# Kernel optimization log

Hardware: AMD Instinct MI355X
Metric: run time of the kernel (lower is better)

## Reference

```python
import jax, jax.numpy as jnp
import numpy as np

D_G, D_2D, D_3D = 512, 768, 1024
D_F, RANK, ATTN_H = 256, 16, 512
B = 8192


def _xavier(key, shape):
    fan_out, fan_in = shape
    lim = float(np.sqrt(6.0 / (fan_in + fan_out)))
    return jax.random.uniform(key, shape, jnp.float32, -lim, lim)


def setup_inputs() -> dict:
    key = jax.random.key(0)
    ks = jax.random.split(key, 12)
    inp = {
        "h_g": jax.random.normal(ks[0], (B, D_G), jnp.float32),
        "h_2d": jax.random.normal(ks[1], (B, D_2D), jnp.float32),
        "h_3d": jax.random.normal(ks[2], (B, D_3D), jnp.float32),
        # modality projections (torch Linear: y = x @ W.T + b)
        "Wg": _xavier(ks[3], (D_F, D_G)),   "bg": jnp.zeros((D_F,), jnp.float32),
        "W2": _xavier(ks[4], (D_F, D_2D)),  "b2": jnp.zeros((D_F,), jnp.float32),
        "W3": _xavier(ks[5], (D_F, D_3D)),  "b3": jnp.zeros((D_F,), jnp.float32),
        # LayerNorm affine params
        "ln_g_w": jnp.ones((D_F,), jnp.float32),  "ln_g_b": jnp.zeros((D_F,), jnp.float32),
        "ln_2_w": jnp.ones((D_F,), jnp.float32),  "ln_2_b": jnp.zeros((D_F,), jnp.float32),
        "ln_3_w": jnp.ones((D_F,), jnp.float32),  "ln_3_b": jnp.zeros((D_F,), jnp.float32),
        # rank expansions (no bias)
        "U": _xavier(ks[6], (RANK * D_F, D_F)),
        "V": _xavier(ks[7], (RANK * D_F, D_F)),
        "S": _xavier(ks[8], (RANK * D_F, D_F)),
        # attention MLP
        "Wa1": _xavier(ks[9], (ATTN_H, D_G + D_2D + D_3D)), "ba1": jnp.zeros((ATTN_H,), jnp.float32),
        "Wa2": _xavier(ks[10], (RANK, ATTN_H)),             "ba2": jnp.zeros((RANK,), jnp.float32),
    }
    return inp


def _layernorm(x, w, b, eps=1e-5):
    mu = jnp.mean(x, axis=-1, keepdims=True)
    var = jnp.var(x, axis=-1, keepdims=True)
    return (x - mu) * jax.lax.rsqrt(var + eps) * w + b


def reference(h_g, h_2d, h_3d, Wg, bg, W2, b2, W3, b3,
              ln_g_w, ln_g_b, ln_2_w, ln_2_b, ln_3_w, ln_3_b,
              U, V, S, Wa1, ba1, Wa2, ba2):
    # proj + LN + ReLU (dropout=0 / eval mode)
    g = jax.nn.relu(_layernorm(h_g @ Wg.T + bg, ln_g_w, ln_g_b))
    d2 = jax.nn.relu(_layernorm(h_2d @ W2.T + b2, ln_2_w, ln_2_b))
    d3 = jax.nn.relu(_layernorm(h_3d @ W3.T + b3, ln_3_w, ln_3_b))
    b = g.shape[0]
    # rank expansion: (B, R, d_f)
    g_r = (g @ U.T).reshape(b, RANK, D_F)
    d2_r = (d2 @ V.T).reshape(b, RANK, D_F)
    d3_r = (d3 @ S.T).reshape(b, RANK, D_F)
    z_r = g_r * d2_r * d3_r  # elementwise tri-linear product
    # rank attention from raw modality concat
    h_cat = jnp.concatenate([h_g, h_2d, h_3d], axis=-1)
    beta = jax.nn.softmax(jax.nn.relu(h_cat @ Wa1.T + ba1) @ Wa2.T + ba2, axis=-1)  # (B, R)
    z = jnp.einsum('brd,br->bd', z_r, beta)  # (B, d_f)
    return z
```

## Files before the change

kernel.cpp:

```cpp
#include <hip/hip_runtime.h>
#include <stdint.h>

#define B_ROWS 8192
#define DG 512
#define D2 768
#define D3 1024
#define DCAT 2304
#define DF 256
#define RANK 16
#define AH 512

#define OFF_WG 0
#define OFF_W2 131072
#define OFF_W3 327680
#define OFF_U  589824
#define OFF_V  1638400
#define OFF_S  2686976
#define OFF_WA1 3735552

#define WS_WBUF  0u
#define WS_GBUF  9830400u
#define WS_A1P   22413312u
#define WS_ZPART 22413312u
#define WS_BETA  55967744u
#define WS_REQUIRED 94240768u

typedef __attribute__((ext_vector_type(8))) short short8;
typedef __attribute__((ext_vector_type(4))) float f32x4;

__device__ inline unsigned short f2bf(float f) {
  union { float f; unsigned int u; } v; v.f = f;
  unsigned int u = v.u + 0x7fffu + ((v.u >> 16) & 1u);
  return (unsigned short)(u >> 16);
}
__device__ inline float bf2f(unsigned short h) {
  union { float f; unsigned int u; } v; v.u = ((unsigned int)h) << 16;
  return v.f;
}

typedef const unsigned int __attribute__((address_space(1)))* as1_u32p;
typedef unsigned int __attribute__((address_space(3)))* as3_u32p;

__device__ inline void g2l16(const unsigned short* g, unsigned short* l) {
  __builtin_amdgcn_global_load_lds((as1_u32p)g, (as3_u32p)l, 16, 0, 0);
}


__global__ __launch_bounds__(256) void cvt_w_k(const float* __restrict__ Wg,
                                               const float* __restrict__ W2,
                                               const float* __restrict__ W3,
                                               const float* __restrict__ U,
                                               const float* __restrict__ V,
                                               const float* __restrict__ S,
                                               const float* __restrict__ Wa1,
                                               unsigned short* __restrict__ wbuf) {
  const int e = (blockIdx.x * 256 + threadIdx.x) * 4;
  const float* src;
  if (e < OFF_W2)       src = Wg  + e;
  else if (e < OFF_W3)  src = W2  + (e - OFF_W2);
  else if (e < OFF_U)   src = W3  + (e - OFF_W3);
  else if (e < OFF_V)   src = U   + (e - OFF_U);
  else if (e < OFF_S)   src = V   + (e - OFF_V);
  else if (e < OFF_WA1) src = S   + (e - OFF_S);
  else                  src = Wa1 + (e - OFF_WA1);
  float4 v = *(const float4*)src;
  ushort4 o;
  o.x = f2bf(v.x); o.y = f2bf(v.y); o.z = f2bf(v.z); o.w = f2bf(v.w);
  *(ushort4*)(wbuf + e) = o;
}


__global__ __launch_bounds__(512, 2) void fatgemm256_k(const float* __restrict__ hgf,
                                                       const float* __restrict__ h2f,
                                                       const float* __restrict__ h3f,
                                                       const unsigned short* __restrict__ wbuf,
                                                       const float* __restrict__ bg,
                                                       const float* __restrict__ b2,
                                                       const float* __restrict__ b3,
                                                       const float* __restrict__ wg,
                                                       const float* __restrict__ wbg,
                                                       const float* __restrict__ w2,
                                                       const float* __restrict__ wb2,
                                                       const float* __restrict__ w3,
                                                       const float* __restrict__ wb3,
                                                       unsigned short* __restrict__ gout,
                                                       unsigned short* __restrict__ a1part) {
  __shared__ __align__(16) unsigned short lA[2 * 256 * 64];
  __shared__ __align__(16) unsigned short lB[2 * 256 * 64];
  const int bid = blockIdx.x;
  const int tid = threadIdx.x;
  const int lane = tid & 63;
  const int wid = tid >> 6;
  const int wr = wid >> 2;
  const int wc = wid & 3;
  const int row_s = tid >> 3;
  const int kc_s = (((tid & 7) ^ (row_s & 7)) << 3);
  const int mbase = wr * 128 + (lane & 15);
  const int nbase = wc * 64 + (lane & 15);
  const int kq = lane >> 4;
  const int h = lane & 7;

  int role_a1 = 0, half = 0, m0 = 0, n0 = 0, z = 0, nt = 0;
  if (bid < 128)      { role_a1 = 1; half = bid >> 6; int r6 = bid & 63;
                        n0 = (r6 & 1) << 8; m0 = (r6 >> 1) << 8; nt = 18; }
  else if (bid < 160) { z = 2; m0 = (bid - 128) << 8; nt = 16; }
  else if (bid < 192) { z = 1; m0 = (bid - 160) << 8; nt = 12; }
  else                { z = 0; m0 = (bid - 192) << 8; nt = 8; }

  const float* projA = (z == 0) ? hgf : ((z == 1) ? h2f : h3f);
  const int Kz   = (z == 0) ? DG : ((z == 1) ? D2 : D3);
  const int woff = (z == 0) ? OFF_WG : ((z == 1) ? OFF_W2 : OFF_W3);

  float4 ar[8];
  auto loadA = [&](int t) {
    const float* Ag; int lda; int ka;
    if (role_a1) {
      const int tt = half * 18 + t;
      if (tt < 8)       { Ag = hgf; lda = DG; ka = tt * 64; }
      else if (tt < 20) { Ag = h2f; lda = D2; ka = (tt - 8) * 64; }
      else              { Ag = h3f; lda = D3; ka = (tt - 20) * 64; }
      Ag += (size_t)m0 * lda;
    } else {
      lda = Kz; Ag = projA + (size_t)m0 * lda; ka = t * 64;
    }
#pragma unroll
    for (int q = 0; q < 4; ++q) {
      const float* src = Ag + (size_t)(q * 64 + row_s) * lda + ka + kc_s;
      ar[q * 2]     = *(const float4*)src;
      ar[q * 2 + 1] = *(const float4*)(src + 4);
    }
  };

  auto writeA = [&](unsigned short* dA) {
#pragma unroll
    for (int q = 0; q < 4; ++q) {
      const float4 a = ar[q * 2], b = ar[q * 2 + 1];
      short8 w;
      w[0] = (short)f2bf(a.x); w[1] = (short)f2bf(a.y);
      w[2] = (short)f2bf(a.z); w[3] = (short)f2bf(a.w);
      w[4] = (short)f2bf(b.x); w[5] = (short)f2bf(b.y);
      w[6] = (short)f2bf(b.z); w[7] = (short)f2bf(b.w);
      *(short8*)(dA + (q * 512 + tid) * 8) = w;
    }
  };

  auto stageB = [&](int t, unsigned short* dB) {
    const unsigned short* Bg; int ldb; int kb;
    if (role_a1) {
      const int tt = half * 18 + t;
      Bg = wbuf + OFF_WA1 + (size_t)n0 * DCAT; ldb = DCAT; kb = tt * 64;
    } else {
      Bg = wbuf + woff; ldb = Kz; kb = t * 64;
    }
#pragma unroll
    for (int q = 0; q < 4; ++q)
      g2l16(Bg + (size_t)(q * 64 + row_s) * ldb + kb + kc_s, dB + (q * 512 + tid) * 8);
  };

  f32x4 acc[8][4];
#pragma unroll
  for (int ti = 0; ti < 8; ++ti)
#pragma unroll
    for (int tj = 0; tj < 4; ++tj)
      acc[ti][tj] = (f32x4){0.f, 0.f, 0.f, 0.f};

  auto compute = [&](const unsigned short* sA, const unsigned short* sB) {
#pragma unroll
    for (int kk = 0; kk < 2; ++kk) {
      const int kch = (kk << 2) + kq;
      const int ko = ((kch ^ h) << 3);
      short8 af[8], bfr[4];
#pragma unroll
      for (int t4 = 0; t4 < 8; ++t4)
        af[t4] = *(const short8*)(sA + (mbase + t4 * 16) * 64 + ko);
#pragma unroll
      for (int t4 = 0; t4 < 4; ++t4)
        bfr[t4] = *(const short8*)(sB + (nbase + t4 * 16) * 64 + ko);
      __builtin_amdgcn_s_setprio(1);
#pragma unroll
      for (int ti = 0; ti < 8; ++ti)
#pragma unroll
        for (int tj = 0; tj < 4; ++tj)
          acc[ti][tj] = __builtin_amdgcn_mfma_f32_16x16x32_bf16(af[ti], bfr[tj], acc[ti][tj], 0, 0, 0);
      __builtin_amdgcn_s_setprio(0);
    }
  };

  stageB(0, lB);
  loadA(0);
  stageB(1, lB + 16384);

  for (int t = 0; t < nt; ++t) {
    const int b = t & 1;
    unsigned short* cA = lA + b * 16384;
    unsigned short* cB = lB + b * 16384;
    if (t + 1 < nt) asm volatile("s_waitcnt vmcnt(4)" ::: "memory");
    else            asm volatile("s_waitcnt vmcnt(0)" ::: "memory");
    __builtin_amdgcn_sched_barrier(0);
    writeA(cA);
    if (t + 1 < nt) loadA(t + 1);
    asm volatile("s_waitcnt lgkmcnt(0)" ::: "memory");
    __builtin_amdgcn_s_barrier();
    __builtin_amdgcn_sched_barrier(0);
    compute(cA, cB);
    __builtin_amdgcn_sched_barrier(0);
    __builtin_amdgcn_s_barrier();
    if (t + 2 < nt) stageB(t + 2, cB);
  }

  if (role_a1) {
    unsigned short* out = a1part + (size_t)half * (B_ROWS * AH);
    const int r0 = m0 + wr * 128 + ((lane >> 4) << 2);
    const int c0 = n0 + wc * 64 + (lane & 15);
#pragma unroll
    for (int ti = 0; ti < 8; ++ti)
#pragma unroll
      for (int tj = 0; tj < 4; ++tj)
#pragma unroll
        for (int i = 0; i < 4; ++i)
          out[(size_t)(r0 + ti * 16 + i) * AH + (c0 + tj * 16)] = f2bf(acc[ti][tj][i]);
  } else {
    const float* bias = (z == 0) ? bg : ((z == 1) ? b2 : b3);
    const float* lnw  = (z == 0) ? wg : ((z == 1) ? w2 : w3);
    const float* lnb  = (z == 0) ? wbg : ((z == 1) ? wb2 : wb3);
    const int cbase = wc * 64 + (lane & 15);
    float bs[4], lw4[4], lb4[4];
#pragma unroll
    for (int tj = 0; tj < 4; ++tj) {
      const int col = cbase + tj * 16;
      bs[tj] = bias[col]; lw4[tj] = lnw[col]; lb4[tj] = lnb[col];
    }
#pragma unroll
    for (int ti = 0; ti < 8; ++ti)
#pragma unroll
      for (int tj = 0; tj < 4; ++tj)
#pragma unroll
        for (int i = 0; i < 4; ++i)
          acc[ti][tj][i] += bs[tj];

    float* lnr = (float*)lA;
    __syncthreads();
#pragma unroll
    for (int ti = 0; ti < 8; ++ti)
#pragma unroll
      for (int i = 0; i < 4; ++i) {
        float s = acc[ti][0][i] + acc[ti][1][i] + acc[ti][2][i] + acc[ti][3][i];
        float q = acc[ti][0][i] * acc[ti][0][i] + acc[ti][1][i] * acc[ti][1][i]
                + acc[ti][2][i] * acc[ti][2][i] + acc[ti][3][i] * acc[ti][3][i];
#pragma unroll
        for (int m = 1; m < 16; m <<= 1) { s += __shfl_xor(s, m, 64); q += __shfl_xor(q, m, 64); }
        if ((lane & 15) == 0) {
          const int rl = wr * 128 + ti * 16 + ((lane >> 4) << 2) + i;
          lnr[rl * 8 + wc * 2]     = s;
          lnr[rl * 8 + wc * 2 + 1] = q;
        }
      }
    __syncthreads();
    unsigned short* gz = gout + (size_t)z * (B_ROWS * DF);
#pragma unroll
    for (int ti = 0; ti < 8; ++ti)
#pragma unroll
      for (int i = 0; i < 4; ++i) {
        const int rl = wr * 128 + ti * 16 + ((lane >> 4) << 2) + i;
        const float4 pa = *(const float4*)(lnr + rl * 8);
        const float4 pb = *(const float4*)(lnr + rl * 8 + 4);
        const float sum = pa.x + pa.z + pb.x + pb.z;
        const float sq  = pa.y + pa.w + pb.y + pb.w;
        const float mean = sum * (1.f / DF);
        const float var  = sq * (1.f / DF) - mean * mean;
        const float rs   = rsqrtf(var + 1e-5f);
        const size_t rowoff = (size_t)(m0 + rl) * DF;
#pragma unroll
        for (int tj = 0; tj < 4; ++tj) {
          const float v = (acc[ti][tj][i] - mean) * rs * lw4[tj] + lb4[tj];
          gz[rowoff + cbase + tj * 16] = f2bf(fmaxf(v, 0.f));
        }
      }
  }
}


__global__ __launch_bounds__(256, 2) void rank_fused_k(const unsigned short* __restrict__ gbuf,
                                                       const unsigned short* __restrict__ wbuf,
                                                       const float* __restrict__ beta,
                                                       float* __restrict__ zpart) {
  __shared__ __align__(16) unsigned short lA[2 * 128 * 64];
  __shared__ __align__(16) unsigned short lB[2 * 128 * 64];
  __shared__ float lbeta[4 * 128];
  const int m0 = blockIdx.x * 128;
  const int d0 = blockIdx.y * 128;
  const int rg = blockIdx.z * 4;
  const int tid = threadIdx.x;

  for (int i = tid; i < 512; i += 256) {
    const int rr = i >> 7, row = i & 127;
    lbeta[i] = beta[(size_t)(m0 + row) * RANK + rg + rr];
  }
  __syncthreads();

  const int lane = tid & 63;
  const int wr = tid >> 7, wc = (tid >> 6) & 1;
  const int row_s = tid >> 3;
  const int kc_s = (((tid & 7) ^ ((tid >> 3) & 7)) << 3);
  const int mbase = wr * 64 + (lane & 15);
  const int nbase = wc * 64 + (lane & 15);
  const int kq = lane >> 4;
  const int h = lane & 7;
  const int lr0 = wr * 64 + ((lane >> 4) << 2);

  const unsigned short* Abase = gbuf + (size_t)(m0 + row_s) * DF + kc_s;
  const unsigned short* Bbase = wbuf + OFF_U + (size_t)(rg * 256 + d0 + row_s) * DF + kc_s;

  auto stage = [&](int t, unsigned short* dA, unsigned short* dB) {
    const int p = t >> 2, ks = t & 3;
    const int rr = p / 3;
    const int zi = p - rr * 3;
    const unsigned short* Ag = Abase + (size_t)zi * (B_ROWS * DF) + ks * 64;
    const unsigned short* Bg = Bbase + (size_t)zi * 1048576 + (size_t)rr * (256 * DF) + ks * 64;
#pragma unroll
    for (int q = 0; q < 4; ++q) {
      const int lofs = (q * 256 + tid) * 8;
      g2l16(Ag + (size_t)q * 32 * DF, dA + lofs);
      g2l16(Bg + (size_t)q * 32 * DF, dB + lofs);
    }
  };

  f32x4 zacc[4][4], prod[4][4], acc[4][4];
#pragma unroll
  for (int ti = 0; ti < 4; ++ti)
#pragma unroll
    for (int tj = 0; tj < 4; ++tj) {
      zacc[ti][tj] = (f32x4){0.f, 0.f, 0.f, 0.f};
      acc[ti][tj]  = (f32x4){0.f, 0.f, 0.f, 0.f};
    }

  auto compute = [&](const unsigned short* sA, const unsigned short* sB) {
#pragma unroll
    for (int kk = 0; kk < 2; ++kk) {
      const int kch = (kk << 2) + kq;
      const int ko = ((kch ^ h) << 3);
      short8 af[4], bfr[4];
#pragma unroll
      for (int t4 = 0; t4 < 4; ++t4) {
        af[t4]  = *(const short8*)(sA + (mbase + t4 * 16) * 64 + ko);
        bfr[t4] = *(const short8*)(sB + (nbase + t4 * 16) * 64 + ko);
      }
      __builtin_amdgcn_s_setprio(1);
#pragma unroll
      for (int ti = 0; ti < 4; ++ti)
#pragma unroll
        for (int tj = 0; tj < 4; ++tj)
          acc[ti][tj] = __builtin_amdgcn_mfma_f32_16x16x32_bf16(af[ti], bfr[tj], acc[ti][tj], 0, 0, 0);
      __builtin_amdgcn_s_setprio(0);
    }
  };

  stage(0, lA, lB);
  stage(1, lA + 8192, lB + 8192);

  for (int p = 0; p < 12; ++p) {
    const int rr = p / 3;
    const int zi = p - rr * 3;
#pragma unroll
    for (int ks = 0; ks < 4; ++ks) {
      const int t = (p << 2) + ks;
      const int b = t & 1;
      unsigned short* cA = lA + b * 8192;
      unsigned short* cB = lB + b * 8192;
      if (t < 47) asm volatile("s_waitcnt vmcnt(8)" ::: "memory");
      else        asm volatile("s_waitcnt vmcnt(0)" ::: "memory");
      __builtin_amdgcn_s_barrier();
      __builtin_amdgcn_sched_barrier(0);
      compute(cA, cB);
      __builtin_amdgcn_sched_barrier(0);
      __builtin_amdgcn_s_barrier();
      if (t + 2 < 48) stage(t + 2, cA, cB);
    }

    if (zi == 0) {
#pragma unroll
      for (int ti = 0; ti < 4; ++ti)
#pragma unroll
        for (int tj = 0; tj < 4; ++tj)
          prod[ti][tj] = acc[ti][tj];
    } else if (zi == 1) {
#pragma unroll
      for (int ti = 0; ti < 4; ++ti)
#pragma unroll
        for (int tj = 0; tj < 4; ++tj)
          prod[ti][tj] *= acc[ti][tj];
    } else {
#pragma unroll
      for (int ti = 0; ti < 4; ++ti) {
        const float4 b4 = *(const float4*)(lbeta + rr * 128 + lr0 + ti * 16);
        const float bv[4] = {b4.x, b4.y, b4.z, b4.w};
#pragma unroll
        for (int tj = 0; tj < 4; ++tj)
#pragma unroll
          for (int i = 0; i < 4; ++i)
            zacc[ti][tj][i] += prod[ti][tj][i] * acc[ti][tj][i] * bv[i];
      }
    }
#pragma unroll
    for (int ti = 0; ti < 4; ++ti)
#pragma unroll
      for (int tj = 0; tj < 4; ++tj)
        acc[ti][tj] = (f32x4){0.f, 0.f, 0.f, 0.f};
  }

  float* zp = zpart + (size_t)blockIdx.z * (B_ROWS * DF);
  const int c0 = d0 + wc * 64 + (lane & 15);
#pragma unroll
  for (int ti = 0; ti < 4; ++ti)
#pragma unroll
    for (int tj = 0; tj < 4; ++tj)
#pragma unroll
      for (int i = 0; i < 4; ++i)
        zp[(size_t)(m0 + lr0 + ti * 16 + i) * DF + (c0 + tj * 16)] = zacc[ti][tj][i];
}


__global__ __launch_bounds__(256) void zsum_k(const float* __restrict__ zpart,
                                              float* __restrict__ z) {
  const int idx = blockIdx.x * 256 + threadIdx.x;
  const size_t e = (size_t)idx * 4;
  const size_t stride = (size_t)B_ROWS * DF;
  float4 a = *(const float4*)(zpart + e);
  float4 b = *(const float4*)(zpart + stride + e);
  float4 c = *(const float4*)(zpart + 2 * stride + e);
  float4 d = *(const float4*)(zpart + 3 * stride + e);
  float4 o;
  o.x = (a.x + b.x) + (c.x + d.x);
  o.y = (a.y + b.y) + (c.y + d.y);
  o.z = (a.z + b.z) + (c.z + d.z);
  o.w = (a.w + b.w) + (c.w + d.w);
  *(float4*)(z + e) = o;
}


__global__ __launch_bounds__(256) void post_beta_k(const unsigned short* __restrict__ a1part,
                                                   const float* __restrict__ ba1,
                                                   const float* __restrict__ Wa2,
                                                   const float* __restrict__ ba2,
                                                   float* __restrict__ beta) {
  __shared__ float lw[RANK * AH];
  for (int i = threadIdx.x; i < RANK * AH / 4; i += 256)
    *(float4*)(lw + i * 4) = *(const float4*)(Wa2 + i * 4);
  __syncthreads();
  const int row = blockIdx.x * 4 + (threadIdx.x >> 6);
  const int lane = threadIdx.x & 63;
  const unsigned short* h0 = a1part + (size_t)row * AH + lane * 8;
  const unsigned short* h1 = h0 + (size_t)B_ROWS * AH;
  const uint4 p0 = *(const uint4*)h0;
  const uint4 p1 = *(const uint4*)h1;
  const unsigned int u0[4] = {p0.x, p0.y, p0.z, p0.w};
  const unsigned int u1[4] = {p1.x, p1.y, p1.z, p1.w};
  float4 ca = *(const float4*)(ba1 + lane * 8);
  float4 cb = *(const float4*)(ba1 + lane * 8 + 4);
  const float bias[8] = {ca.x, ca.y, ca.z, ca.w, cb.x, cb.y, cb.z, cb.w};
  float av[8];
#pragma unroll
  for (int j = 0; j < 4; ++j) {
    const float s0 = bf2f((unsigned short)(u0[j] & 0xffffu)) + bf2f((unsigned short)(u1[j] & 0xffffu));
    const float s1 = bf2f((unsigned short)(u0[j] >> 16)) + bf2f((unsigned short)(u1[j] >> 16));
    av[2 * j]     = fmaxf(s0 + bias[2 * j], 0.f);
    av[2 * j + 1] = fmaxf(s1 + bias[2 * j + 1], 0.f);
  }
  float lg[RANK];
#pragma unroll
  for (int r = 0; r < RANK; ++r) {
    const float* wrow = lw + r * AH + lane * 8;
    float4 wa = *(const float4*)wrow;
    float4 wb = *(const float4*)(wrow + 4);
    float p = av[0] * wa.x + av[1] * wa.y + av[2] * wa.z + av[3] * wa.w
            + av[4] * wb.x + av[5] * wb.y + av[6] * wb.z + av[7] * wb.w;
#pragma unroll
    for (int m = 1; m < 64; m <<= 1) p += __shfl_xor(p, m, 64);
    lg[r] = p + ba2[r];
  }
  float mx = lg[0];
#pragma unroll
  for (int r = 1; r < RANK; ++r) mx = fmaxf(mx, lg[r]);
  float den = 0.f;
#pragma unroll
  for (int r = 0; r < RANK; ++r) { lg[r] = __expf(lg[r] - mx); den += lg[r]; }
  const float inv = 1.f / den;
  if (lane < RANK) {
    float mine = 0.f;
#pragma unroll
    for (int r = 0; r < RANK; ++r) mine = (lane == r) ? lg[r] : mine;
    beta[(size_t)row * RANK + lane] = mine * inv;
  }
}


extern "C" void kernel_launch(void* const* d_in, const int* in_sizes, int n_in,
                              void* d_out, int out_size, void* d_ws, size_t ws_size,
                              hipStream_t stream) {
  if (ws_size < (size_t)WS_REQUIRED) return;

  const float* h_g   = (const float*)d_in[0];
  const float* h_2d  = (const float*)d_in[1];
  const float* h_3d  = (const float*)d_in[2];
  const float* Wg    = (const float*)d_in[3];
  const float* bg    = (const float*)d_in[4];
  const float* W2    = (const float*)d_in[5];
  const float* b2    = (const float*)d_in[6];
  const float* W3    = (const float*)d_in[7];
  const float* b3    = (const float*)d_in[8];
  const float* ln_g_w = (const float*)d_in[9];
  const float* ln_g_b = (const float*)d_in[10];
  const float* ln_2_w = (const float*)d_in[11];
  const float* ln_2_b = (const float*)d_in[12];
  const float* ln_3_w = (const float*)d_in[13];
  const float* ln_3_b = (const float*)d_in[14];
  const float* U     = (const float*)d_in[15];
  const float* V     = (const float*)d_in[16];
  const float* S     = (const float*)d_in[17];
  const float* Wa1   = (const float*)d_in[18];
  const float* ba1   = (const float*)d_in[19];
  const float* Wa2   = (const float*)d_in[20];
  const float* ba2   = (const float*)d_in[21];

  char* ws = (char*)d_ws;
  unsigned short* wbuf   = (unsigned short*)(ws + WS_WBUF);
  unsigned short* gbuf   = (unsigned short*)(ws + WS_GBUF);
  unsigned short* a1part = (unsigned short*)(ws + WS_A1P);
  float*          zpart  = (float*)(ws + WS_ZPART);
  float*          beta   = (float*)(ws + WS_BETA);
  float* z = (float*)d_out;

  cvt_w_k<<<dim3(4800), dim3(256), 0, stream>>>(Wg, W2, W3, U, V, S, Wa1, wbuf);
  fatgemm256_k<<<dim3(224), dim3(512), 0, stream>>>(h_g, h_2d, h_3d, wbuf,
                                                    bg, b2, b3,
                                                    ln_g_w, ln_g_b, ln_2_w, ln_2_b,
                                                    ln_3_w, ln_3_b,
                                                    gbuf, a1part);
  post_beta_k<<<dim3(2048), dim3(256), 0, stream>>>(a1part, ba1, Wa2, ba2, beta);
  rank_fused_k<<<dim3(64, 2, 4), dim3(256), 0, stream>>>(gbuf, wbuf, beta, zpart);
  zsum_k<<<dim3(2048), dim3(256), 0, stream>>>(zpart, z);
}
```

Baseline: 287.0 us.

## Overlap U/V/S bf16 conversion with projection GEMM and deepen A prefetch

```diff
diff --git a/kernel.cpp b/kernel.cpp
--- a/kernel.cpp
+++ b/kernel.cpp
@@ -49,31 +49,30 @@
 __global__ __launch_bounds__(256) void cvt_w_k(const float* __restrict__ Wg,
                                                const float* __restrict__ W2,
                                                const float* __restrict__ W3,
-                                               const float* __restrict__ U,
-                                               const float* __restrict__ V,
-                                               const float* __restrict__ S,
                                                const float* __restrict__ Wa1,
                                                unsigned short* __restrict__ wbuf) {
   const int e = (blockIdx.x * 256 + threadIdx.x) * 4;
   const float* src;
-  if (e < OFF_W2)       src = Wg  + e;
-  else if (e < OFF_W3)  src = W2  + (e - OFF_W2);
-  else if (e < OFF_U)   src = W3  + (e - OFF_W3);
-  else if (e < OFF_V)   src = U   + (e - OFF_U);
-  else if (e < OFF_S)   src = V   + (e - OFF_V);
-  else if (e < OFF_WA1) src = S   + (e - OFF_S);
-  else                  src = Wa1 + (e - OFF_WA1);
+  unsigned short* dst;
+  if (e < OFF_W2)      { src = Wg + e;             dst = wbuf + e; }
+  else if (e < OFF_W3) { src = W2 + (e - OFF_W2);  dst = wbuf + e; }
+  else if (e < OFF_U)  { src = W3 + (e - OFF_W3);  dst = wbuf + e; }
+  else                 { src = Wa1 + (e - OFF_U);  dst = wbuf + OFF_WA1 + (e - OFF_U); }
   float4 v = *(const float4*)src;
   ushort4 o;
   o.x = f2bf(v.x); o.y = f2bf(v.y); o.z = f2bf(v.z); o.w = f2bf(v.w);
-  *(ushort4*)(wbuf + e) = o;
+  *(ushort4*)dst = o;
 }
 
 
 __global__ __launch_bounds__(512, 2) void fatgemm256_k(const float* __restrict__ hgf,
                                                        const float* __restrict__ h2f,
                                                        const float* __restrict__ h3f,
+                                                       const float* __restrict__ U,
+                                                       const float* __restrict__ V,
+                                                       const float* __restrict__ S,
                                                        const unsigned short* __restrict__ wbuf,
+                                                       unsigned short* __restrict__ wbuf_uvs,
                                                        const float* __restrict__ bg,
                                                        const float* __restrict__ b2,
                                                        const float* __restrict__ b3,
@@ -85,10 +84,27 @@
                                                        const float* __restrict__ wb3,
                                                        unsigned short* __restrict__ gout,
                                                        unsigned short* __restrict__ a1part) {
+  const int bid = blockIdx.x;
+  const int tid = threadIdx.x;
+
+  if (bid >= 224) {
+    const int t0 = (bid - 224) * 512 + tid;
+    for (int i = 0; i < 48; ++i) {
+      const size_t e = ((size_t)(t0 + i * 16384)) * 4;
+      const float* src;
+      if (e < 1048576)      src = U + e;
+      else if (e < 2097152) src = V + (e - 1048576);
+      else                  src = S + (e - 2097152);
+      float4 v = *(const float4*)src;
+      ushort4 o;
+      o.x = f2bf(v.x); o.y = f2bf(v.y); o.z = f2bf(v.z); o.w = f2bf(v.w);
+      *(ushort4*)(wbuf_uvs + OFF_U + e) = o;
+    }
+    return;
+  }
+
   __shared__ __align__(16) unsigned short lA[2 * 256 * 64];
   __shared__ __align__(16) unsigned short lB[2 * 256 * 64];
-  const int bid = blockIdx.x;
-  const int tid = threadIdx.x;
   const int lane = tid & 63;
   const int wid = tid >> 6;
   const int wr = wid >> 2;
@@ -111,8 +127,7 @@
   const int Kz   = (z == 0) ? DG : ((z == 1) ? D2 : D3);
   const int woff = (z == 0) ? OFF_WG : ((z == 1) ? OFF_W2 : OFF_W3);
 
-  float4 ar[8];
-  auto loadA = [&](int t) {
+  auto loadA = [&](float4 (&ar)[8], int t) {
     const float* Ag; int lda; int ka;
     if (role_a1) {
       const int tt = half * 18 + t;
@@ -131,7 +146,7 @@
     }
   };
 
-  auto writeA = [&](unsigned short* dA) {
+  auto writeA = [&](const float4 (&ar)[8], unsigned short* dA) {
 #pragma unroll
     for (int q = 0; q < 4; ++q) {
       const float4 a = ar[q * 2], b = ar[q * 2 + 1];
@@ -186,26 +201,36 @@
     }
   };
 
+  float4 arA[8], arB[8];
+  loadA(arA, 0);
   stageB(0, lB);
-  loadA(0);
+  loadA(arB, 1);
   stageB(1, lB + 16384);
 
-  for (int t = 0; t < nt; ++t) {
-    const int b = t & 1;
-    unsigned short* cA = lA + b * 16384;
-    unsigned short* cB = lB + b * 16384;
-    if (t + 1 < nt) asm volatile("s_waitcnt vmcnt(4)" ::: "memory");
-    else            asm volatile("s_waitcnt vmcnt(0)" ::: "memory");
+  for (int t = 0; t < nt; t += 2) {
+    asm volatile("s_waitcnt vmcnt(12)" ::: "memory");
     __builtin_amdgcn_sched_barrier(0);
-    writeA(cA);
-    if (t + 1 < nt) loadA(t + 1);
+    writeA(arA, lA);
+    if (t + 2 < nt) loadA(arA, t + 2);
     asm volatile("s_waitcnt lgkmcnt(0)" ::: "memory");
     __builtin_amdgcn_s_barrier();
     __builtin_amdgcn_sched_barrier(0);
-    compute(cA, cB);
+    compute(lA, lB);
     __builtin_amdgcn_sched_barrier(0);
     __builtin_amdgcn_s_barrier();
-    if (t + 2 < nt) stageB(t + 2, cB);
+    if (t + 2 < nt) stageB(t + 2, lB);
+    if (t + 3 < nt) asm volatile("s_waitcnt vmcnt(12)" ::: "memory");
+    else            asm volatile("s_waitcnt vmcnt(0)" ::: "memory");
+    __builtin_amdgcn_sched_barrier(0);
+    writeA(arB, lA + 16384);
+    if (t + 3 < nt) loadA(arB, t + 3);
+    asm volatile("s_waitcnt lgkmcnt(0)" ::: "memory");
+    __builtin_amdgcn_s_barrier();
+    __builtin_amdgcn_sched_barrier(0);
+    compute(lA + 16384, lB + 16384);
+    __builtin_amdgcn_sched_barrier(0);
+    __builtin_amdgcn_s_barrier();
+    if (t + 3 < nt) stageB(t + 3, lB + 16384);
   }
 
   if (role_a1) {
@@ -530,8 +555,8 @@
   float*          beta   = (float*)(ws + WS_BETA);
   float* z = (float*)d_out;
 
-  cvt_w_k<<<dim3(4800), dim3(256), 0, stream>>>(Wg, W2, W3, U, V, S, Wa1, wbuf);
-  fatgemm256_k<<<dim3(224), dim3(512), 0, stream>>>(h_g, h_2d, h_3d, wbuf,
+  cvt_w_k<<<dim3(1728), dim3(256), 0, stream>>>(Wg, W2, W3, Wa1, wbuf);
+  fatgemm256_k<<<dim3(256), dim3(512), 0, stream>>>(h_g, h_2d, h_3d, U, V, S, wbuf, wbuf,
                                                     bg, b2, b3,
                                                     ln_g_w, ln_g_b, ln_2_w, ln_2_b,
                                                     ln_3_w, ln_3_b,
```

Measured after the change: 396.4 us. +38.1%, slower.

## Overlap U/V/S bf16 conversion with projection GEMM using extra blocks

Applied to the files above, without the earlier changes.

```diff
diff --git a/kernel.cpp b/kernel.cpp
--- a/kernel.cpp
+++ b/kernel.cpp
@@ -49,31 +49,30 @@
 __global__ __launch_bounds__(256) void cvt_w_k(const float* __restrict__ Wg,
                                                const float* __restrict__ W2,
                                                const float* __restrict__ W3,
-                                               const float* __restrict__ U,
-                                               const float* __restrict__ V,
-                                               const float* __restrict__ S,
                                                const float* __restrict__ Wa1,
                                                unsigned short* __restrict__ wbuf) {
   const int e = (blockIdx.x * 256 + threadIdx.x) * 4;
   const float* src;
-  if (e < OFF_W2)       src = Wg  + e;
-  else if (e < OFF_W3)  src = W2  + (e - OFF_W2);
-  else if (e < OFF_U)   src = W3  + (e - OFF_W3);
-  else if (e < OFF_V)   src = U   + (e - OFF_U);
-  else if (e < OFF_S)   src = V   + (e - OFF_V);
-  else if (e < OFF_WA1) src = S   + (e - OFF_S);
-  else                  src = Wa1 + (e - OFF_WA1);
+  unsigned short* dst;
+  if (e < OFF_W2)      { src = Wg + e;             dst = wbuf + e; }
+  else if (e < OFF_W3) { src = W2 + (e - OFF_W2);  dst = wbuf + e; }
+  else if (e < OFF_U)  { src = W3 + (e - OFF_W3);  dst = wbuf + e; }
+  else                 { src = Wa1 + (e - OFF_U);  dst = wbuf + OFF_WA1 + (e - OFF_U); }
   float4 v = *(const float4*)src;
   ushort4 o;
   o.x = f2bf(v.x); o.y = f2bf(v.y); o.z = f2bf(v.z); o.w = f2bf(v.w);
-  *(ushort4*)(wbuf + e) = o;
+  *(ushort4*)dst = o;
 }
 
 
 __global__ __launch_bounds__(512, 2) void fatgemm256_k(const float* __restrict__ hgf,
                                                        const float* __restrict__ h2f,
                                                        const float* __restrict__ h3f,
+                                                       const float* __restrict__ U,
+                                                       const float* __restrict__ V,
+                                                       const float* __restrict__ S,
                                                        const unsigned short* __restrict__ wbuf,
+                                                       unsigned short* __restrict__ wbuf_uvs,
                                                        const float* __restrict__ bg,
                                                        const float* __restrict__ b2,
                                                        const float* __restrict__ b3,
@@ -85,10 +84,27 @@
                                                        const float* __restrict__ wb3,
                                                        unsigned short* __restrict__ gout,
                                                        unsigned short* __restrict__ a1part) {
+  const int bid = blockIdx.x;
+  const int tid = threadIdx.x;
+
+  if (bid >= 224) {
+    const int t0 = (bid - 224) * 512 + tid;
+    for (int i = 0; i < 48; ++i) {
+      const size_t e = ((size_t)(t0 + i * 16384)) * 4;
+      const float* src;
+      if (e < 1048576)      src = U + e;
+      else if (e < 2097152) src = V + (e - 1048576);
+      else                  src = S + (e - 2097152);
+      float4 v = *(const float4*)src;
+      ushort4 o;
+      o.x = f2bf(v.x); o.y = f2bf(v.y); o.z = f2bf(v.z); o.w = f2bf(v.w);
+      *(ushort4*)(wbuf_uvs + OFF_U + e) = o;
+    }
+    return;
+  }
+
   __shared__ __align__(16) unsigned short lA[2 * 256 * 64];
   __shared__ __align__(16) unsigned short lB[2 * 256 * 64];
-  const int bid = blockIdx.x;
-  const int tid = threadIdx.x;
   const int lane = tid & 63;
   const int wid = tid >> 6;
   const int wr = wid >> 2;
@@ -530,8 +546,8 @@
   float*          beta   = (float*)(ws + WS_BETA);
   float* z = (float*)d_out;
 
-  cvt_w_k<<<dim3(4800), dim3(256), 0, stream>>>(Wg, W2, W3, U, V, S, Wa1, wbuf);
-  fatgemm256_k<<<dim3(224), dim3(512), 0, stream>>>(h_g, h_2d, h_3d, wbuf,
+  cvt_w_k<<<dim3(1728), dim3(256), 0, stream>>>(Wg, W2, W3, Wa1, wbuf);
+  fatgemm256_k<<<dim3(256), dim3(512), 0, stream>>>(h_g, h_2d, h_3d, U, V, S, wbuf, wbuf,
                                                     bg, b2, b3,
                                                     ln_g_w, ln_g_b, ln_2_w, ln_2_b,
                                                     ln_3_w, ln_3_b,
```

Result: no change. 286.6 us, median of 2 (-0.1%).
